# Kernel optimization log

Hardware: AMD Instinct MI355X
Metric: run time of the kernel (lower is better)

Reference implementation:

```python
import jax, jax.numpy as jnp
import numpy as np

EMP = 0.1       # threshold from init
EPS = 1e-8      # torch.cosine_similarity eps
ZERO = 9e-15    # replacement value below threshold


def setup_inputs() -> dict:
    key = jax.random.key(0)
    k1, k2 = jax.random.split(key)
    B, N, F = 4, 4096, 64
    x = jax.random.normal(k1, (B, N, F), dtype=jnp.float32)
    w = jax.random.normal(k2, (1, N, F), dtype=jnp.float32)
    return {"x": x, "w": w}


def reference(x, w):
    # x: (B, N, F); w: (1, N, F)
    xw = x * w
    # cosine similarity via normalize + matmul (torch eps clamp on norms)
    nrm = jnp.maximum(jnp.sqrt(jnp.sum(xw * xw, axis=-1, keepdims=True)), EPS)
    xn = xw / nrm                                  # (B, N, F)
    cos = jnp.einsum('bif,bjf->bij', xn, xn)       # (B, N, N)
    return jnp.where(cos > EMP, cos, jnp.asarray(ZERO, cos.dtype))
```

## Files before the change

kernel.cpp:

```cpp
#include <hip/hip_runtime.h>
#include <hip/hip_bf16.h>

typedef _Float16 f16x8 __attribute__((ext_vector_type(8)));
typedef float f32x4 __attribute__((ext_vector_type(4)));

#define N_ROWS 4096
#define F_DIM 64
#define BATCH 4
#define EMPF 0.1f
#define EMPD 0.1
#define ZEROV 9e-15f
#define WINDOW 2e-4f
#define REG_CAP 256u
#define N_BLOCKS 4096

__global__ __launch_bounds__(256) void normalize_split_kernel(
    const float* __restrict__ x, const float* __restrict__ w,
    _Float16* __restrict__ hi, _Float16* __restrict__ lo) {
  const int lane = threadIdx.x & 63;
  const int wid = threadIdx.x >> 6;
  const int rg = blockIdx.x * 4 + wid;
  const int n = rg & (N_ROWS - 1);
  const float xv = x[rg * F_DIM + lane];
  const float wv = w[n * F_DIM + lane];
  const float p = xv * wv;
  float s = p * p;
#pragma unroll
  for (int off = 32; off >= 1; off >>= 1) s += __shfl_xor(s, off, 64);
  const float nrm = fmaxf(sqrtf(s), 1e-8f);
  const float xn = p / nrm;
  const _Float16 h = (_Float16)xn;
  const float rem = xn - (float)h;
  hi[rg * F_DIM + lane] = h;
  lo[rg * F_DIM + lane] = (_Float16)rem;
}

__global__ __launch_bounds__(256) void gram_kernel(
    const _Float16* __restrict__ hi, const _Float16* __restrict__ lo,
    float* __restrict__ out, unsigned* __restrict__ cnt,
    unsigned* __restrict__ regions) {
  __shared__ unsigned lds_cnt;
  if (threadIdx.x == 0) lds_cnt = 0;
  __syncthreads();

  const int lane = threadIdx.x & 63;
  const int wid = threadIdx.x >> 6;
  const int wm = wid >> 1, wn = wid & 1;
  const int b = blockIdx.z;
  const int row0 = blockIdx.x * 128 + wm * 64;
  const int col0 = blockIdx.y * 128 + wn * 64;
  const int rbase = b * N_ROWS;
  const unsigned bid =
      ((unsigned)blockIdx.z * gridDim.y + blockIdx.y) * gridDim.x + blockIdx.x;
  unsigned* __restrict__ region = regions + (size_t)bid * REG_CAP;

  const int lr = lane & 15;
  const int lk = (lane >> 4) * 8;

  f32x4 acc[4][4] = {};

#pragma unroll
  for (int kf = 0; kf < 2; ++kf) {
    f16x8 ah[4], al[4], bh[4], bl[4];
#pragma unroll
    for (int i = 0; i < 4; ++i) {
      const int ra = (rbase + row0 + i * 16 + lr) * F_DIM + kf * 32 + lk;
      ah[i] = *(const f16x8*)(hi + ra);
      al[i] = *(const f16x8*)(lo + ra);
      const int rb = (rbase + col0 + i * 16 + lr) * F_DIM + kf * 32 + lk;
      bh[i] = *(const f16x8*)(hi + rb);
      bl[i] = *(const f16x8*)(lo + rb);
    }
#pragma unroll
    for (int i = 0; i < 4; ++i) {
#pragma unroll
      for (int j = 0; j < 4; ++j) {
        acc[i][j] = __builtin_amdgcn_mfma_f32_16x16x32_f16(bh[j], ah[i], acc[i][j], 0, 0, 0);
        acc[i][j] = __builtin_amdgcn_mfma_f32_16x16x32_f16(bh[j], al[i], acc[i][j], 0, 0, 0);
        acc[i][j] = __builtin_amdgcn_mfma_f32_16x16x32_f16(bl[j], ah[i], acc[i][j], 0, 0, 0);
      }
    }
  }

  const int r_in = lane & 15;
  const int cb = (lane >> 4) * 4;
#pragma unroll
  for (int i = 0; i < 4; ++i) {
#pragma unroll
    for (int j = 0; j < 4; ++j) {
      f32x4 v = acc[i][j];
      const int row = row0 + i * 16 + r_in;
      const int col = col0 + j * 16 + cb;
#pragma unroll
      for (int r = 0; r < 4; ++r) {
        const float e = v[r];
        if (fabsf(e - EMPF) < WINDOW) {
          const unsigned pos = atomicAdd(&lds_cnt, 1u);
          if (pos < REG_CAP)
            region[pos] = ((unsigned)b << 24) | ((unsigned)row << 12) | (unsigned)(col + r);
        }
        v[r] = (e > EMPF) ? e : ZEROV;
      }
      const size_t oi = ((size_t)b << 24) + ((size_t)row << 12) + (size_t)col;
      *(f32x4*)(out + oi) = v;
    }
  }

  __syncthreads();
  if (threadIdx.x == 0) cnt[bid] = lds_cnt < REG_CAP ? lds_cnt : REG_CAP;
}

__global__ __launch_bounds__(256) void refine_kernel(
    const float* __restrict__ x, const float* __restrict__ w,
    float* __restrict__ out, const unsigned* __restrict__ cnt,
    const unsigned* __restrict__ regions) {
  const int lane = threadIdx.x & 63;
  const unsigned wg0 = blockIdx.x * (blockDim.x >> 6) + (threadIdx.x >> 6);
  const unsigned nw = gridDim.x * (blockDim.x >> 6);
  for (unsigned rgn = wg0; rgn < N_BLOCKS; rgn += nw) {
    const unsigned count = cnt[rgn];
    const unsigned* __restrict__ region = regions + (size_t)rgn * REG_CAP;
    for (unsigned e = 0; e < count; ++e) {
      const unsigned ent = region[e];
      const int b = (int)(ent >> 24);
      const int i = (int)((ent >> 12) & 4095);
      const int j = (int)(ent & 4095);
      const double wi = (double)w[i * F_DIM + lane];
      const double wj = (double)w[j * F_DIM + lane];
      const double xi = (double)x[(b * N_ROWS + i) * F_DIM + lane];
      const double xj = (double)x[(b * N_ROWS + j) * F_DIM + lane];
      const double pi = xi * wi;
      const double pj = xj * wj;
      double si = pi * pi, sj = pj * pj, sij = pi * pj;
#pragma unroll
      for (int off = 32; off >= 1; off >>= 1) {
        si += __shfl_xor(si, off, 64);
        sj += __shfl_xor(sj, off, 64);
        sij += __shfl_xor(sij, off, 64);
      }
      if (lane == 0) {
        const double ni = fmax(sqrt(si), 1e-8);
        const double nj = fmax(sqrt(sj), 1e-8);
        const double c = sij / (ni * nj);
        const double res = (c > EMPD) ? c : (double)ZEROV;
        out[((size_t)b << 24) + ((size_t)i << 12) + (size_t)j] = (float)res;
      }
    }
  }
}

extern "C" void kernel_launch(void* const* d_in, const int* in_sizes, int n_in,
                              void* d_out, int out_size, void* d_ws, size_t ws_size,
                              hipStream_t stream) {
  const float* x = (const float*)d_in[0];
  const float* w = (const float*)d_in[1];
  float* out = (float*)d_out;

  char* ws = (char*)d_ws;
  _Float16* hi = (_Float16*)ws;
  _Float16* lo = (_Float16*)(ws + (size_t)16384 * 64 * 2);
  unsigned* cnt = (unsigned*)(ws + (size_t)4 * 1024 * 1024);
  unsigned* regions = (unsigned*)(ws + (size_t)4 * 1024 * 1024 + 16384);

  normalize_split_kernel<<<4096, 256, 0, stream>>>(x, w, hi, lo);
  gram_kernel<<<dim3(32, 32, 4), 256, 0, stream>>>(hi, lo, out, cnt, regions);
  refine_kernel<<<1024, 256, 0, stream>>>(x, w, out, cnt, regions);
}
```

Before: 133.2 us.

## Stream gram tile by column strip to cut accumulator registers and branch epilogue

The gram kernel now keeps only the A-side hi/lo fragments resident and loops over the four 16-column strips one at a time. Each strip gets a fresh 4-accumulator set and its results are stored right after computing, instead of holding a 4x4 accumulator array. This lowers register pressure to allow more waves and interleaves stores with MFMA work. The near-threshold check is also made wave-uniform with __any so the atomic logging path is skipped when no lane needs it. The trade-off is that the non-unrolled j loop serialises B loads against MFMAs within a wave.

```diff
diff --git a/kernel.cpp b/kernel.cpp
--- a/kernel.cpp
+++ b/kernel.cpp
@@ -57,50 +57,57 @@
   const int lr = lane & 15;
   const int lk = (lane >> 4) * 8;
 
-  f32x4 acc[4][4] = {};
-
+  f16x8 ah[2][4], al[2][4];
 #pragma unroll
-  for (int kf = 0; kf < 2; ++kf) {
-    f16x8 ah[4], al[4], bh[4], bl[4];
+  for (int kf = 0; kf < 2; ++kf)
 #pragma unroll
     for (int i = 0; i < 4; ++i) {
       const int ra = (rbase + row0 + i * 16 + lr) * F_DIM + kf * 32 + lk;
-      ah[i] = *(const f16x8*)(hi + ra);
-      al[i] = *(const f16x8*)(lo + ra);
-      const int rb = (rbase + col0 + i * 16 + lr) * F_DIM + kf * 32 + lk;
-      bh[i] = *(const f16x8*)(hi + rb);
-      bl[i] = *(const f16x8*)(lo + rb);
+      ah[kf][i] = *(const f16x8*)(hi + ra);
+      al[kf][i] = *(const f16x8*)(lo + ra);
+    }
+
+  const int r_in = lane & 15;
+  const int cb = (lane >> 4) * 4;
+
+#pragma unroll 1
+  for (int j = 0; j < 4; ++j) {
+    f16x8 bh[2], bl[2];
+#pragma unroll
+    for (int kf = 0; kf < 2; ++kf) {
+      const int rb = (rbase + col0 + j * 16 + lr) * F_DIM + kf * 32 + lk;
+      bh[kf] = *(const f16x8*)(hi + rb);
+      bl[kf] = *(const f16x8*)(lo + rb);
+    }
+    f32x4 acc[4] = {};
+#pragma unroll
+    for (int i = 0; i < 4; ++i) {
+#pragma unroll
+      for (int kf = 0; kf < 2; ++kf) {
+        acc[i] = __builtin_amdgcn_mfma_f32_16x16x32_f16(bh[kf], ah[kf][i], acc[i], 0, 0, 0);
+        acc[i] = __builtin_amdgcn_mfma_f32_16x16x32_f16(bh[kf], al[kf][i], acc[i], 0, 0, 0);
+        acc[i] = __builtin_amdgcn_mfma_f32_16x16x32_f16(bl[kf], ah[kf][i], acc[i], 0, 0, 0);
+      }
     }
 #pragma unroll
     for (int i = 0; i < 4; ++i) {
-#pragma unroll
-      for (int j = 0; j < 4; ++j) {
-        acc[i][j] = __builtin_amdgcn_mfma_f32_16x16x32_f16(bh[j], ah[i], acc[i][j], 0, 0, 0);
-        acc[i][j] = __builtin_amdgcn_mfma_f32_16x16x32_f16(bh[j], al[i], acc[i][j], 0, 0, 0);
-        acc[i][j] = __builtin_amdgcn_mfma_f32_16x16x32_f16(bl[j], ah[i], acc[i][j], 0, 0, 0);
-      }
-    }
-  }
-
-  const int r_in = lane & 15;
-  const int cb = (lane >> 4) * 4;
-#pragma unroll
-  for (int i = 0; i < 4; ++i) {
-#pragma unroll
-    for (int j = 0; j < 4; ++j) {
-      f32x4 v = acc[i][j];
+      f32x4 v = acc[i];
       const int row = row0 + i * 16 + r_in;
       const int col = col0 + j * 16 + cb;
+      const bool near = fabsf(v[0] - EMPF) < WINDOW || fabsf(v[1] - EMPF) < WINDOW ||
+                        fabsf(v[2] - EMPF) < WINDOW || fabsf(v[3] - EMPF) < WINDOW;
+      if (__builtin_expect(__any((int)near), 0)) {
 #pragma unroll
-      for (int r = 0; r < 4; ++r) {
-        const float e = v[r];
-        if (fabsf(e - EMPF) < WINDOW) {
-          const unsigned pos = atomicAdd(&lds_cnt, 1u);
-          if (pos < REG_CAP)
-            region[pos] = ((unsigned)b << 24) | ((unsigned)row << 12) | (unsigned)(col + r);
+        for (int r = 0; r < 4; ++r) {
+          if (fabsf(v[r] - EMPF) < WINDOW) {
+            const unsigned pos = atomicAdd(&lds_cnt, 1u);
+            if (pos < REG_CAP)
+              region[pos] = ((unsigned)b << 24) | ((unsigned)row << 12) | (unsigned)(col + r);
+          }
         }
-        v[r] = (e > EMPF) ? e : ZEROV;
       }
+#pragma unroll
+      for (int r = 0; r < 4; ++r) v[r] = (v[r] > EMPF) ? v[r] : ZEROV;
       const size_t oi = ((size_t)b << 24) + ((size_t)row << 12) + (size_t)col;
       *(f32x4*)(out + oi) = v;
     }
```

Measured after the change: 130.7 us. No clear change (-1.9%).
